# Kernel tuning notes

Hardware: AMD Instinct MI355X
Metric: run time of the kernel (lower is better)

The kernel has to match this reference:

```python
import jax, jax.numpy as jnp
import numpy as np

EPS = 1e-12  # torch F.normalize eps


def _row_normalize(x):
    # torch.nn.functional.normalize(x, p=2, dim=-1)
    n = jnp.linalg.norm(x, axis=-1, keepdims=True)
    return x / jnp.maximum(n, EPS)


def _word_pool(word_emb, ids, mask):
    # [B, L, D] gather -> per-word L2 normalize -> mean over valid words
    e = _row_normalize(word_emb[ids])
    m = mask.astype(e.dtype)[..., None]  # [B, L, 1]
    cnt = jnp.maximum(m.sum(axis=1), 1.0)
    return (e * m).sum(axis=1) / cnt  # [B, D]


def setup_inputs() -> dict:
    key = jax.random.key(0)
    ks = jax.random.split(key, 12)
    NE, NR, NW, D = 500000, 1000, 100000, 60
    B, L = 65536, 24
    init = 0.001
    inp = {
        "ent_emb": init * jax.random.normal(ks[0], (NE, D), jnp.float32),
        "rel_emb": init * jax.random.normal(ks[1], (NR, D), jnp.float32),
        "word_emb": init * jax.random.normal(ks[2], (NW, D), jnp.float32),
        "e_bias": init * jax.random.normal(ks[3], (NE, 1), jnp.float32),
        "r_bias": init * jax.random.normal(ks[4], (NR, 1), jnp.float32),
        "head": jax.random.randint(ks[5], (B,), 0, NE, jnp.int32),
        "relation": jax.random.randint(ks[6], (B,), 0, NR, jnp.int32),
        "tail": jax.random.randint(ks[7], (B,), 0, NE, jnp.int32),
        "head_w": jax.random.randint(ks[8], (B, L), 0, NW, jnp.int32),
        "rel_w": jax.random.randint(ks[9], (B, L), 0, NW, jnp.int32),
        "tail_w": jax.random.randint(ks[10], (B, L), 0, NW, jnp.int32),
    }
    mk = jax.random.split(ks[11], 3)
    for name, k in zip(["head_w_mask", "rel_w_mask", "tail_w_mask"], mk):
        m = jax.random.randint(k, (B, L), 0, 2, jnp.int32)
        inp[name] = m.at[:, 0].set(1)  # ensure every ragged list is non-empty
    return inp


def reference(ent_emb, rel_emb, word_emb, e_bias, r_bias,
              head, relation, tail,
              head_w, rel_w, tail_w,
              head_w_mask, rel_w_mask, tail_w_mask):
    head_e = _row_normalize(ent_emb[head])
    rel_e = _row_normalize(rel_emb[relation])
    tail_e = _row_normalize(ent_emb[tail])

    head_e = head_e + _word_pool(word_emb, head_w, head_w_mask)
    rel_e = rel_e + _word_pool(word_emb, rel_w, rel_w_mask)
    tail_e = tail_e + _word_pool(word_emb, tail_w, tail_w_mask)

    score = -jnp.linalg.norm(head_e + rel_e - tail_e, axis=1)
    score = score + e_bias[head, 0] + e_bias[tail, 0] + r_bias[relation, 0]
    return score
```

## Files before the change

kernel.cpp:

```cpp
#include <hip/hip_runtime.h>
#include <hip/hip_bf16.h>

#define NORM_EPS 1e-12f
#define D 60
#define RP 64
#define L 24
#define SSTR 28
#define ITEM_STRIDE 768
#define BIAS_OFF 336
#define ROWS_OFF 384

__device__ __forceinline__ float wave_sum(float v) {
    #pragma unroll
    for (int off = 32; off >= 1; off >>= 1)
        v += __shfl_xor(v, off, 64);
    return v;
}

__device__ __forceinline__ int rfl(int x) { return __builtin_amdgcn_readfirstlane(x); }

__device__ __forceinline__ float bf2f(unsigned short u) {
    unsigned x = (unsigned)u << 16;
    float f;
    __builtin_memcpy(&f, &x, 4);
    return f;
}

__device__ __forceinline__ unsigned pack_bf16(float a, float b) {
    __hip_bfloat16 lo = __float2bfloat16(a);
    __hip_bfloat16 hi = __float2bfloat16(b);
    unsigned short ul, uh;
    __builtin_memcpy(&ul, &lo, 2);
    __builtin_memcpy(&uh, &hi, 2);
    return (unsigned)ul | ((unsigned)uh << 16);
}

__global__ __launch_bounds__(256) void norm_bf16_tab_kernel(
    const float* __restrict__ emb, __hip_bfloat16* __restrict__ outw, int N, int zrow)
{
    int row = (int)(blockIdx.x * blockDim.x + threadIdx.x);
    if (row >= N + zrow) return;

    uint4* dst = (uint4*)(outw + (size_t)row * RP);
    if (row == N) {
        uint4 z = make_uint4(0u, 0u, 0u, 0u);
        #pragma unroll
        for (int j = 0; j < 8; ++j) dst[j] = z;
        return;
    }

    const float4* src = (const float4*)(emb + (size_t)row * D);
    float4 v[15];
    #pragma unroll
    for (int i = 0; i < 15; ++i) v[i] = src[i];

    float ss = 0.f;
    #pragma unroll
    for (int i = 0; i < 15; ++i)
        ss += v[i].x * v[i].x + v[i].y * v[i].y + v[i].z * v[i].z + v[i].w * v[i].w;
    float inv = 1.f / fmaxf(sqrtf(ss), NORM_EPS);

    float f[60];
    #pragma unroll
    for (int i = 0; i < 15; ++i) {
        f[4*i+0] = v[i].x * inv; f[4*i+1] = v[i].y * inv;
        f[4*i+2] = v[i].z * inv; f[4*i+3] = v[i].w * inv;
    }
    unsigned w[32];
    #pragma unroll
    for (int i = 0; i < 30; ++i) w[i] = pack_bf16(f[2*i], f[2*i+1]);
    w[30] = 0u; w[31] = 0u;

    #pragma unroll
    for (int j = 0; j < 8; ++j)
        dst[j] = make_uint4(w[4*j+0], w[4*j+1], w[4*j+2], w[4*j+3]);
}

__device__ __forceinline__ void write_norm_row(const float* __restrict__ src,
                                               char* __restrict__ dst)
{
    const float4* s4 = (const float4*)src;
    float4 v[15];
    #pragma unroll
    for (int i = 0; i < 15; ++i) v[i] = s4[i];
    float ss = 0.f;
    #pragma unroll
    for (int i = 0; i < 15; ++i)
        ss += v[i].x * v[i].x + v[i].y * v[i].y + v[i].z * v[i].z + v[i].w * v[i].w;
    float inv = 1.f / fmaxf(sqrtf(ss), NORM_EPS);
    float f[60];
    #pragma unroll
    for (int i = 0; i < 15; ++i) {
        f[4*i+0] = v[i].x * inv; f[4*i+1] = v[i].y * inv;
        f[4*i+2] = v[i].z * inv; f[4*i+3] = v[i].w * inv;
    }
    unsigned w[32];
    #pragma unroll
    for (int i = 0; i < 30; ++i) w[i] = pack_bf16(f[2*i], f[2*i+1]);
    w[30] = 0u; w[31] = 0u;
    uint4* d4 = (uint4*)dst;
    #pragma unroll
    for (int j = 0; j < 8; ++j)
        d4[j] = make_uint4(w[4*j+0], w[4*j+1], w[4*j+2], w[4*j+3]);
}

__global__ __launch_bounds__(256) void prep_kernel(
    const float* __restrict__ ent_emb, const float* __restrict__ rel_emb,
    const float* __restrict__ e_bias, const float* __restrict__ r_bias,
    const int* __restrict__ head, const int* __restrict__ relation,
    const int* __restrict__ tail,
    const int* __restrict__ hw, const int* __restrict__ rw, const int* __restrict__ tw,
    const int* __restrict__ hm, const int* __restrict__ rm, const int* __restrict__ tm,
    char* __restrict__ blob, int B, int NW)
{
    int b = (int)(blockIdx.x * blockDim.x + threadIdx.x);
    if (b >= B) return;

    char* ob = blob + (size_t)b * ITEM_STRIDE;

    const int* idp[3] = { hw, rw, tw };
    const int* mkp[3] = { hm, rm, tm };
    int* o = (int*)ob;
    #pragma unroll
    for (int s = 0; s < 3; ++s) {
        const int4* ip = (const int4*)(idp[s] + (size_t)b * L);
        const int4* mp = (const int4*)(mkp[s] + (size_t)b * L);
        int cnt = 0;
        int4* ov = (int4*)o;
        #pragma unroll
        for (int i = 0; i < L / 4; ++i) {
            int4 ti = ip[i];
            int4 tm4 = mp[i];
            int4 so;
            so.x = tm4.x ? ti.x : NW; cnt += (tm4.x ? 1 : 0);
            so.y = tm4.y ? ti.y : NW; cnt += (tm4.y ? 1 : 0);
            so.z = tm4.z ? ti.z : NW; cnt += (tm4.z ? 1 : 0);
            so.w = tm4.w ? ti.w : NW; cnt += (tm4.w ? 1 : 0);
            ov[i] = so;
        }
        float invc = 1.f / (float)(cnt > 0 ? cnt : 1);
        ov[6] = make_int4(__float_as_int(invc), 0, 0, 0);
        o += SSTR;
    }

    int h = head[b];
    int r = relation[b];
    int t = tail[b];
    float bias = e_bias[h] + e_bias[t] + r_bias[r];
    *(float*)(ob + BIAS_OFF) = bias;

    write_norm_row(ent_emb + (size_t)h * D, ob + ROWS_OFF);
    write_norm_row(rel_emb + (size_t)r * D, ob + ROWS_OFF + 128);
    write_norm_row(ent_emb + (size_t)t * D, ob + ROWS_OFF + 256);
}

__global__ __launch_bounds__(256) void score_kernel_v8(
    const __hip_bfloat16* __restrict__ wt,
    const char* __restrict__ blob,
    float* __restrict__ out,
    int B)
{
    int wid = (int)((blockIdx.x * (unsigned)blockDim.x + threadIdx.x) >> 6);
    int lane = (int)(threadIdx.x & 63u);
    if (wid >= B) return;
    int b = rfl(wid);

    int d = lane;
    unsigned doff2 = (unsigned)(((d < D) ? d : 0) * 2);

    const char* ob = blob + (size_t)b * ITEM_STRIDE;
    const char* wtb = (const char*)wt;

    const int4* sb = (const int4*)ob;
    int4 q[21];
    #pragma unroll
    for (int i = 0; i < 21; ++i) q[i] = sb[i];

    unsigned off[72];
    #pragma unroll
    for (int s = 0; s < 3; ++s) {
        #pragma unroll
        for (int i = 0; i < 6; ++i) {
            int4 ti = q[s * 7 + i];
            int base = s * 24 + 4 * i;
            off[base + 0] = ((unsigned)ti.x << 7) + doff2;
            off[base + 1] = ((unsigned)ti.y << 7) + doff2;
            off[base + 2] = ((unsigned)ti.z << 7) + doff2;
            off[base + 3] = ((unsigned)ti.w << 7) + doff2;
        }
    }

    unsigned short raw[72];
    #pragma unroll
    for (int j = 0; j < 72; ++j)
        raw[j] = *(const unsigned short*)(wtb + off[j]);
    unsigned short rawh = *(const unsigned short*)(ob + ROWS_OFF + doff2);
    unsigned short rawr = *(const unsigned short*)(ob + ROWS_OFF + 128 + doff2);
    unsigned short rawt = *(const unsigned short*)(ob + ROWS_OFF + 256 + doff2);
    float bias = *(const float*)(ob + BIAS_OFF);

    float pool[3];
    #pragma unroll
    for (int s = 0; s < 3; ++s) {
        float s0 = 0.f, s1 = 0.f, s2 = 0.f, s3 = 0.f;
        #pragma unroll
        for (int l = 0; l < L; l += 4) {
            s0 += bf2f(raw[s * 24 + l + 0]);
            s1 += bf2f(raw[s * 24 + l + 1]);
            s2 += bf2f(raw[s * 24 + l + 2]);
            s3 += bf2f(raw[s * 24 + l + 3]);
        }
        float acc = (s0 + s1) + (s2 + s3);
        pool[s] = acc * __int_as_float(q[s * 7 + 6].x);
    }

    float vh = bf2f(rawh);
    float vr = bf2f(rawr);
    float vt = bf2f(rawt);

    float comb = (vh + pool[0]) + (vr + pool[1]) - (vt + pool[2]);
    comb = (d < D) ? comb : 0.f;
    float nsc = sqrtf(wave_sum(comb * comb));

    float score = -nsc + bias;
    if (lane == 0) out[wid] = score;
}

__device__ __forceinline__ float word_pool_slow(const float* __restrict__ word_emb,
                                                const int* __restrict__ ids,
                                                const int* __restrict__ mask,
                                                int b, int d, bool act)
{
    float acc = 0.f;
    int cnt = 0;
    #pragma unroll
    for (int l = 0; l < L; ++l) {
        int m = mask[b * L + l];
        if (m) {
            int id = ids[b * L + l];
            float v = act ? word_emb[(size_t)id * D + d] : 0.f;
            float n = sqrtf(wave_sum(v * v));
            acc += v / fmaxf(n, NORM_EPS);
            cnt += 1;
        }
    }
    return acc / (float)(cnt > 0 ? cnt : 1);
}

__global__ __launch_bounds__(256) void transe_score_slow_kernel(
    const float* __restrict__ ent_emb, const float* __restrict__ rel_emb,
    const float* __restrict__ word_emb, const float* __restrict__ e_bias,
    const float* __restrict__ r_bias,
    const int* __restrict__ head, const int* __restrict__ relation,
    const int* __restrict__ tail,
    const int* __restrict__ head_w, const int* __restrict__ rel_w,
    const int* __restrict__ tail_w,
    const int* __restrict__ head_m, const int* __restrict__ rel_m,
    const int* __restrict__ tail_m,
    float* __restrict__ out, int B)
{
    int wid = (int)((blockIdx.x * (unsigned)blockDim.x + threadIdx.x) >> 6);
    int lane = (int)(threadIdx.x & 63u);
    if (wid >= B) return;
    int d = lane;
    bool act = d < D;

    int h = head[wid], r = relation[wid], t = tail[wid];

    float vh = act ? ent_emb[(size_t)h * D + d] : 0.f;
    float vr = act ? rel_emb[(size_t)r * D + d] : 0.f;
    float vt = act ? ent_emb[(size_t)t * D + d] : 0.f;
    vh /= fmaxf(sqrtf(wave_sum(vh * vh)), NORM_EPS);
    vr /= fmaxf(sqrtf(wave_sum(vr * vr)), NORM_EPS);
    vt /= fmaxf(sqrtf(wave_sum(vt * vt)), NORM_EPS);

    float ph = word_pool_slow(word_emb, head_w, head_m, wid, d, act);
    float pr = word_pool_slow(word_emb, rel_w,  rel_m,  wid, d, act);
    float pt = word_pool_slow(word_emb, tail_w, tail_m, wid, d, act);

    float comb = (vh + ph) + (vr + pr) - (vt + pt);
    float nsc = sqrtf(wave_sum(comb * comb));
    float score = -nsc + e_bias[h] + e_bias[t] + r_bias[r];
    if (lane == 0) out[wid] = score;
}

extern "C" void kernel_launch(void* const* d_in, const int* in_sizes, int n_in,
                              void* d_out, int out_size, void* d_ws, size_t ws_size,
                              hipStream_t stream) {
    const float* ent_emb  = (const float*)d_in[0];
    const float* rel_emb  = (const float*)d_in[1];
    const float* word_emb = (const float*)d_in[2];
    const float* e_bias   = (const float*)d_in[3];
    const float* r_bias   = (const float*)d_in[4];
    const int*   head     = (const int*)d_in[5];
    const int*   relation = (const int*)d_in[6];
    const int*   tail     = (const int*)d_in[7];
    const int*   head_w   = (const int*)d_in[8];
    const int*   rel_w    = (const int*)d_in[9];
    const int*   tail_w   = (const int*)d_in[10];
    const int*   head_m   = (const int*)d_in[11];
    const int*   rel_m    = (const int*)d_in[12];
    const int*   tail_m   = (const int*)d_in[13];
    float* out = (float*)d_out;

    int B  = in_sizes[5];
    int NE = in_sizes[0] / D;
    int NR = in_sizes[1] / D;
    int NW = in_sizes[2] / D;
    (void)NE; (void)NR;

    int wpb = 256 / 64;

    size_t wt_bytes   = (size_t)(NW + 1) * RP * sizeof(__hip_bfloat16);
    size_t blob_bytes = (size_t)B * ITEM_STRIDE;
    size_t need = wt_bytes + blob_bytes;

    if (ws_size >= need) {
        __hip_bfloat16* wt = (__hip_bfloat16*)d_ws;
        char* blob = (char*)d_ws + wt_bytes;

        norm_bf16_tab_kernel<<<(NW + 1 + 255) / 256, 256, 0, stream>>>(word_emb, wt, NW, 1);
        prep_kernel<<<(B + 255) / 256, 256, 0, stream>>>(
            ent_emb, rel_emb, e_bias, r_bias,
            head, relation, tail,
            head_w, rel_w, tail_w, head_m, rel_m, tail_m,
            blob, B, NW);

        score_kernel_v8<<<(B + wpb - 1) / wpb, 256, 0, stream>>>(
            wt, blob, out, B);
    } else {
        transe_score_slow_kernel<<<(B + wpb - 1) / wpb, 256, 0, stream>>>(
            ent_emb, rel_emb, word_emb, e_bias, r_bias,
            head, relation, tail,
            head_w, rel_w, tail_w, head_m, rel_m, tail_m, out, B);
    }
}
```

Baseline: 92.41 us.

## Split entity row normalization into a wave-per-row kernel

Moves the gather, normalization and bf16 packing of the head, relation and tail rows out of the thread-per-item prep kernel into a new kernel that gives each row one 64-lane wave with a shuffle reduction. The old path had a single thread read three scattered 240-byte rows, which gives poor coalescing and heavy register use. The new kernel reads coalesced and uses much wider parallelism. The cost is an extra kernel launch and narrow 2-byte stores into the blob.

```diff
diff --git a/kernel.cpp b/kernel.cpp
--- a/kernel.cpp
+++ b/kernel.cpp
@@ -36,10 +36,10 @@
 }
 
 __global__ __launch_bounds__(256) void norm_bf16_tab_kernel(
-    const float* __restrict__ emb, __hip_bfloat16* __restrict__ outw, int N, int zrow)
+    const float* __restrict__ emb, __hip_bfloat16* __restrict__ outw, int N)
 {
     int row = (int)(blockIdx.x * blockDim.x + threadIdx.x);
-    if (row >= N + zrow) return;
+    if (row > N) return;
 
     uint4* dst = (uint4*)(outw + (size_t)row * RP);
     if (row == N) {
@@ -76,36 +76,7 @@
         dst[j] = make_uint4(w[4*j+0], w[4*j+1], w[4*j+2], w[4*j+3]);
 }
 
-__device__ __forceinline__ void write_norm_row(const float* __restrict__ src,
-                                               char* __restrict__ dst)
-{
-    const float4* s4 = (const float4*)src;
-    float4 v[15];
-    #pragma unroll
-    for (int i = 0; i < 15; ++i) v[i] = s4[i];
-    float ss = 0.f;
-    #pragma unroll
-    for (int i = 0; i < 15; ++i)
-        ss += v[i].x * v[i].x + v[i].y * v[i].y + v[i].z * v[i].z + v[i].w * v[i].w;
-    float inv = 1.f / fmaxf(sqrtf(ss), NORM_EPS);
-    float f[60];
-    #pragma unroll
-    for (int i = 0; i < 15; ++i) {
-        f[4*i+0] = v[i].x * inv; f[4*i+1] = v[i].y * inv;
-        f[4*i+2] = v[i].z * inv; f[4*i+3] = v[i].w * inv;
-    }
-    unsigned w[32];
-    #pragma unroll
-    for (int i = 0; i < 30; ++i) w[i] = pack_bf16(f[2*i], f[2*i+1]);
-    w[30] = 0u; w[31] = 0u;
-    uint4* d4 = (uint4*)dst;
-    #pragma unroll
-    for (int j = 0; j < 8; ++j)
-        d4[j] = make_uint4(w[4*j+0], w[4*j+1], w[4*j+2], w[4*j+3]);
-}
-
-__global__ __launch_bounds__(256) void prep_kernel(
-    const float* __restrict__ ent_emb, const float* __restrict__ rel_emb,
+__global__ __launch_bounds__(256) void sanitize_kernel(
     const float* __restrict__ e_bias, const float* __restrict__ r_bias,
     const int* __restrict__ head, const int* __restrict__ relation,
     const int* __restrict__ tail,
@@ -146,12 +117,40 @@
     int h = head[b];
     int r = relation[b];
     int t = tail[b];
-    float bias = e_bias[h] + e_bias[t] + r_bias[r];
-    *(float*)(ob + BIAS_OFF) = bias;
-
-    write_norm_row(ent_emb + (size_t)h * D, ob + ROWS_OFF);
-    write_norm_row(rel_emb + (size_t)r * D, ob + ROWS_OFF + 128);
-    write_norm_row(ent_emb + (size_t)t * D, ob + ROWS_OFF + 256);
+    *(float*)(ob + BIAS_OFF) = e_bias[h] + e_bias[t] + r_bias[r];
+}
+
+__global__ __launch_bounds__(256) void rows_kernel(
+    const float* __restrict__ ent_emb, const float* __restrict__ rel_emb,
+    const int* __restrict__ head, const int* __restrict__ relation,
+    const int* __restrict__ tail,
+    char* __restrict__ blob, int B)
+{
+    unsigned rid = (unsigned)((blockIdx.x * (unsigned)blockDim.x + threadIdx.x) >> 6);
+    int lane = (int)(threadIdx.x & 63u);
+    unsigned nrows = 3u * (unsigned)B;
+    if (rid >= nrows) return;
+
+    unsigned b = rid / 3u;
+    unsigned s = rid - 3u * b;
+
+    int idx;
+    const float* src;
+    if (s == 0)      { idx = head[b];     src = ent_emb; }
+    else if (s == 1) { idx = relation[b]; src = rel_emb; }
+    else             { idx = tail[b];     src = ent_emb; }
+
+    float v = (lane < D) ? src[(size_t)idx * D + lane] : 0.f;
+    float ss = wave_sum(v * v);
+    float inv = 1.f / fmaxf(sqrtf(ss), NORM_EPS);
+
+    __hip_bfloat16 h16 = __float2bfloat16(v * inv);
+    unsigned short u;
+    __builtin_memcpy(&u, &h16, 2);
+    if (lane >= D) u = 0;
+
+    *(unsigned short*)(blob + (size_t)b * ITEM_STRIDE + ROWS_OFF
+                       + (size_t)s * 128 + (size_t)lane * 2) = u;
 }
 
 __global__ __launch_bounds__(256) void score_kernel_v8(
@@ -304,10 +303,7 @@
     float* out = (float*)d_out;
 
     int B  = in_sizes[5];
-    int NE = in_sizes[0] / D;
-    int NR = in_sizes[1] / D;
     int NW = in_sizes[2] / D;
-    (void)NE; (void)NR;
 
     int wpb = 256 / 64;
 
@@ -319,12 +315,14 @@
         __hip_bfloat16* wt = (__hip_bfloat16*)d_ws;
         char* blob = (char*)d_ws + wt_bytes;
 
-        norm_bf16_tab_kernel<<<(NW + 1 + 255) / 256, 256, 0, stream>>>(word_emb, wt, NW, 1);
-        prep_kernel<<<(B + 255) / 256, 256, 0, stream>>>(
-            ent_emb, rel_emb, e_bias, r_bias,
-            head, relation, tail,
+        norm_bf16_tab_kernel<<<(NW + 1 + 255) / 256, 256, 0, stream>>>(word_emb, wt, NW);
+        sanitize_kernel<<<(B + 255) / 256, 256, 0, stream>>>(
+            e_bias, r_bias, head, relation, tail,
             head_w, rel_w, tail_w, head_m, rel_m, tail_m,
             blob, B, NW);
+        unsigned nrows = 3u * (unsigned)B;
+        rows_kernel<<<(nrows + wpb - 1) / wpb, 256, 0, stream>>>(
+            ent_emb, rel_emb, head, relation, tail, blob, B);
 
         score_kernel_v8<<<(B + wpb - 1) / wpb, 256, 0, stream>>>(
             wt, blob, out, B);
```

After: 112.1 us. 1.21x slower.
